# Kernel tuning notes

Hardware: AMD Instinct MI355X
Metric: run time of the kernel (lower is better)

## Reference

```python
import jax, jax.numpy as jnp
import numpy as np
import math


def _cnot_perm(n, c, t):
    # permutation on basis states implementing CNOT(control=c, target=t), qubit 0 = MSB
    idx = np.arange(2 ** n)
    ctrl = (idx >> (n - 1 - c)) & 1
    return np.where(ctrl == 1, idx ^ (1 << (n - 1 - t)), idx)


def _rot(phi, theta, omega):
    # PennyLane Rot(phi, theta, omega) = RZ(omega) RY(theta) RZ(phi)
    c = jnp.cos(theta / 2.0)
    s = jnp.sin(theta / 2.0)
    m00 = jnp.exp(-0.5j * (phi + omega)) * c
    m01 = -jnp.exp(0.5j * (phi - omega)) * s
    m10 = jnp.exp(-0.5j * (phi - omega)) * s
    m11 = jnp.exp(0.5j * (phi + omega)) * c
    return jnp.stack([jnp.stack([m00, m01]), jnp.stack([m10, m11])])


def _apply_1q(state, U, q, n):
    # apply 2x2 gate U on qubit q of an [N, 2^n] statevector
    N = state.shape[0]
    s = state.reshape(N, 2 ** q, 2, 2 ** (n - q - 1))
    s = jnp.einsum('ab,nqbr->nqar', U, s)
    return s.reshape(N, 2 ** n)


def reference(x, weights, bias, filter_size, strides):
    fs, st = int(filter_size), int(strides)
    B, C, H, W = x.shape
    Cout, L, n, _ = weights.shape
    oh = (H - fs) // st + 1
    ow = (W - fs) // st + 1

    # im2col / torch.unfold: [B,C,oh,fs,ow,fs] -> [B,oh,ow,C,fs,fs] -> [N, C*fs*fs]
    rows = (jnp.arange(oh) * st)[:, None] + jnp.arange(fs)[None, :]
    cols = (jnp.arange(ow) * st)[:, None] + jnp.arange(fs)[None, :]
    patches = x[:, :, rows][:, :, :, :, cols]                 # [B,C,oh,fs,ow,fs]
    patches = patches.transpose(0, 2, 4, 1, 3, 5).reshape(B * oh * ow, C * fs * fs)

    D = C * fs * fs
    dim = 2 ** n
    if D < dim:
        patches = jnp.pad(patches, ((0, 0), (0, dim - D)))

    # amplitude-encoding normalization; all-zero patch vectors are masked to 0 output
    norm = jnp.linalg.norm(patches, axis=-1, keepdims=True)
    nonzero = (norm[:, 0] > 0).astype(patches.dtype)          # [N]
    state0 = (patches / jnp.where(norm > 0, norm, 1.0)).astype(jnp.complex64)

    perms = [jnp.asarray(_cnot_perm(n, q, (q + 1) % n)) for q in range(n)]
    sign = (1.0 - 2.0 * ((jnp.arange(dim) >> (n - 1)) & 1)).astype(jnp.float32)  # Z on qubit 0

    def run_channel(wc):  # wc: [L, n, 3]
        state = state0
        for l in range(L):
            for q in range(n):
                state = _apply_1q(state, _rot(wc[l, q, 0], wc[l, q, 1], wc[l, q, 2]), q, n)
            if n > 1:
                for q in range(n):  # CNOT ring
                    state = state[:, perms[q]]
        return jnp.sum((jnp.abs(state) ** 2) * sign, axis=-1)  # [N] expval Z0

    exps = jax.vmap(run_channel)(weights)                     # [Cout, N]
    out = exps * nonzero[None, :] + bias[:, None]
    return out.reshape(Cout, B, oh, ow).transpose(1, 0, 2, 3)


def setup_inputs() -> dict:
    key = jax.random.key(0)
    k1, k2, k3 = jax.random.split(key, 3)
    B, Cin, H, W = 32, 16, 64, 64
    Cout, L, fs, st = 8, 3, 4, 2
    D = Cin * fs * fs
    n = math.ceil(math.log2(D))
    x = jax.random.normal(k1, (B, Cin, H, W), dtype=jnp.float32)
    weights = jax.random.normal(k2, (Cout, L, n, 3), dtype=jnp.float32)
    kk = 1.0 / D
    bias = jax.random.uniform(k3, (Cout,), minval=-math.sqrt(kk), maxval=math.sqrt(kk), dtype=jnp.float32)
    return {"x": x, "weights": weights, "bias": bias, "filter_size": fs, "strides": st}
```

## Files before the change

kernel.cpp:

```cpp
#include <hip/hip_runtime.h>
#include <math.h>

#define NQ     8
#define DIM    256
#define LAYERS 3
#define COUT   8
#define NB     32
#define OH     31
#define OW     31
#define NPATCH (NB*OH*OW)
#define NTILE8 32
#define PTOT   (NTILE8*1024)
#define NPTILE (PTOT/16)
#define NPAIR  72
#define MPACK  (NPAIR*64*8)
#define NWBLK  512

typedef _Float16 f16x8 __attribute__((ext_vector_type(8)));
typedef _Float16 f16x4 __attribute__((ext_vector_type(4)));
typedef _Float16 f16x2 __attribute__((ext_vector_type(2)));
typedef __fp16   h16x2 __attribute__((ext_vector_type(2)));
typedef float    f32x4 __attribute__((ext_vector_type(4)));

__device__ __constant__ unsigned char TI_OF_P[NPAIR] = {
    0,0,0,0,0,0,0,0, 1,1,1,1,1,1,1,1, 2,2,2,2,2,2,2, 3,3,3,3,3,3,3,
    4,4,4,4,4,4, 5,5,5,5,5,5, 6,6,6,6,6, 7,7,7,7,7, 8,8,8,8, 9,9,9,9,
    10,10,10, 11,11,11, 12,12, 13,13, 14, 15};
__device__ __constant__ unsigned char OFFT_C[16] =
    {0,8,16,23,30,36,42,47,52,56,60,63,66,68,70,71};

__device__ __forceinline__ float2 cmul(float2 a, float2 b) {
    return make_float2(a.x*b.x - a.y*b.y, a.x*b.y + a.y*b.x);
}
__device__ __forceinline__ float2 cadd(float2 a, float2 b) {
    return make_float2(a.x + b.x, a.y + b.y);
}

__device__ __forceinline__ int rho(int i) {
    #pragma unroll
    for (int q = 7; q >= 0; --q) {
        int t = (q + 1) & 7;
        if ((i >> (7 - q)) & 1) i ^= 1 << (7 - t);
    }
    return i;
}

__device__ __forceinline__ void gload_lds16(const _Float16* g, _Float16* l) {
    __builtin_amdgcn_global_load_lds(
        (const __attribute__((address_space(1))) void*)g,
        (__attribute__((address_space(3))) void*)l, 16, 0, 0);
}

__device__ __forceinline__ float fold4(f16x4 sv, f32x4 a, float o) {
    h16x2 s01 = __builtin_bit_cast(h16x2, (f16x2)__builtin_shufflevector(sv, sv, 0, 1));
    h16x2 s23 = __builtin_bit_cast(h16x2, (f16x2)__builtin_shufflevector(sv, sv, 2, 3));
    h16x2 y01 = __builtin_amdgcn_cvt_pkrtz(a[0], a[1]);
    h16x2 y23 = __builtin_amdgcn_cvt_pkrtz(a[2], a[3]);
    o = __builtin_amdgcn_fdot2(s01, y01, o, false);
    o = __builtin_amdgcn_fdot2(s23, y23, o, false);
    return o;
}

__device__ __forceinline__ float dpp_ror_add(float x, int ctrl) {
    int xi = __builtin_bit_cast(int, x);
    int yi;
    switch (ctrl) {
        case 0x128: yi = __builtin_amdgcn_update_dpp(0, xi, 0x128, 0xf, 0xf, true); break;
        case 0x124: yi = __builtin_amdgcn_update_dpp(0, xi, 0x124, 0xf, 0xf, true); break;
        case 0x122: yi = __builtin_amdgcn_update_dpp(0, xi, 0x122, 0xf, 0xf, true); break;
        default:    yi = __builtin_amdgcn_update_dpp(0, xi, 0x121, 0xf, 0xf, true); break;
    }
    return x + __builtin_bit_cast(float, yi);
}

__global__ __launch_bounds__(256) void wext(const float* __restrict__ w,
                                            _Float16* __restrict__ At,
                                            _Float16* __restrict__ Bt,
                                            const float* __restrict__ x,
                                            _Float16* __restrict__ sF) {
    __shared__ float2 g[96];
    __shared__ float2 vb[1024];
    __shared__ _Float16 sT[16][264];
    __shared__ float rsums[16][4];

    if (blockIdx.x < NWBLK) {
        const int ch  = blockIdx.x >> 6;
        const int wv  = threadIdx.x >> 6;
        const int l   = threadIdx.x & 63;
        const int col = (blockIdx.x & 63) * 4 + wv;

        if (threadIdx.x < 24) {
            const float* wp = w + (ch*24 + threadIdx.x)*3;
            float phi = wp[0], th = wp[1], om = wp[2];
            float cth = cosf(th * 0.5f), sth = sinf(th * 0.5f);
            float a = 0.5f * (phi + om), b = 0.5f * (phi - om);
            float sa, ca, sb, cb;
            sincosf(a, &sa, &ca);
            sincosf(b, &sb, &cb);
            g[threadIdx.x*4+0] = make_float2( cth*ca, -cth*sa);
            g[threadIdx.x*4+1] = make_float2(-sth*cb, -sth*sb);
            g[threadIdx.x*4+2] = make_float2( sth*cb, -sth*sb);
            g[threadIdx.x*4+3] = make_float2( cth*ca,  cth*sa);
        }
        __syncthreads();

        float2* vcol = vb + wv * 256;
        float2 v[4];
        #pragma unroll
        for (int k = 0; k < 4; ++k) {
            int r = l + 64*k;
            float2 acc = make_float2(1.f, 0.f);
            #pragma unroll
            for (int q = 0; q < 8; ++q) {
                int iq = (r >> (7 - q)) & 1, jq = (col >> (7 - q)) & 1;
                acc = cmul(acc, g[q*4 + iq*2 + jq]);
            }
            v[k] = acc;
        }

        #pragma unroll
        for (int lay = 1; lay < 3; ++lay) {
            #pragma unroll
            for (int k = 0; k < 4; ++k) vcol[l + 64*k] = v[k];
            #pragma unroll
            for (int k = 0; k < 4; ++k) v[k] = vcol[rho(l + 64*k)];
            {
                const float2 g0 = g[(lay*8+0)*4+0], g1 = g[(lay*8+0)*4+1];
                const float2 g2 = g[(lay*8+0)*4+2], g3 = g[(lay*8+0)*4+3];
                float2 nv[4];
                #pragma unroll
                for (int k = 0; k < 4; ++k) {
                    float2 xx = v[k], yy = v[k^2];
                    nv[k] = (k & 2) ? cadd(cmul(g2, yy), cmul(g3, xx))
                                    : cadd(cmul(g0, xx), cmul(g1, yy));
                }
                #pragma unroll
                for (int k = 0; k < 4; ++k) v[k] = nv[k];
            }
            {
                const float2 g0 = g[(lay*8+1)*4+0], g1 = g[(lay*8+1)*4+1];
                const float2 g2 = g[(lay*8+1)*4+2], g3 = g[(lay*8+1)*4+3];
                float2 nv[4];
                #pragma unroll
                for (int k = 0; k < 4; ++k) {
                    float2 xx = v[k], yy = v[k^1];
                    nv[k] = (k & 1) ? cadd(cmul(g2, yy), cmul(g3, xx))
                                    : cadd(cmul(g0, xx), cmul(g1, yy));
                }
                #pragma unroll
                for (int k = 0; k < 4; ++k) v[k] = nv[k];
            }
            #pragma unroll
            for (int q = 2; q < 8; ++q) {
                int bit = 1 << (7 - q);
                const float2 g0 = g[(lay*8+q)*4+0], g1 = g[(lay*8+q)*4+1];
                const float2 g2 = g[(lay*8+q)*4+2], g3 = g[(lay*8+q)*4+3];
                #pragma unroll
                for (int k = 0; k < 4; ++k) {
                    float2 yy;
                    yy.x = __shfl_xor(v[k].x, bit, 64);
                    yy.y = __shfl_xor(v[k].y, bit, 64);
                    float2 m0 = (l & bit) ? g3 : g0;
                    float2 m1 = (l & bit) ? g2 : g1;
                    v[k] = cadd(cmul(m0, v[k]), cmul(m1, yy));
                }
            }
        }
        #pragma unroll
        for (int k = 0; k < 4; ++k) vcol[l + 64*k] = v[k];
        #pragma unroll
        for (int k = 0; k < 4; ++k) v[k] = vcol[rho(l + 64*k)];

        size_t rowb = ((size_t)ch*256 + col) * 512;
        #pragma unroll
        for (int k = 0; k < 4; ++k) {
            int r = l + 64*k;
            float sgn = (r & 128) ? -1.f : 1.f;
            At[rowb + r]       = (_Float16)(sgn * v[k].x);
            At[rowb + 256 + r] = (_Float16)(sgn * v[k].y);
            Bt[rowb + r]       = (_Float16)v[k].x;
            Bt[rowb + 256 + r] = (_Float16)v[k].y;
        }
    } else {
        const int tb  = blockIdx.x - NWBLK;
        const int tid = threadIdx.x;
        const int wv  = tid >> 6, lane = tid & 63;

        float2 va[4], vc[4];
        #pragma unroll
        for (int pp = 0; pp < 4; ++pp) {
            int pl = wv*4 + pp;
            int p  = tb*16 + pl;
            float2 v01 = make_float2(0.f,0.f), v23 = make_float2(0.f,0.f);
            if (p < NPATCH) {
                int b = p / (OH*OW); int r = p % (OH*OW);
                int oi = r / OW, oj = r % OW;
                int ci = lane >> 2, fi = lane & 3;
                const float* xb = x + (((size_t)(b*16 + ci))*64 + (oi*2 + fi))*64 + oj*2;
                v01 = *(const float2*)xb;
                v23 = *(const float2*)(xb + 2);
            }
            va[pp] = v01; vc[pp] = v23;
            float ss = v01.x*v01.x + v01.y*v01.y + v23.x*v23.x + v23.y*v23.y;
            ss = dpp_ror_add(ss, 0x128);
            ss = dpp_ror_add(ss, 0x124);
            ss = dpp_ror_add(ss, 0x122);
            ss = dpp_ror_add(ss, 0x121);
            if ((lane & 15) == 0) rsums[pl][lane >> 4] = ss;
        }
        __syncthreads();

        #pragma unroll
        for (int pp = 0; pp < 4; ++pp) {
            int pl = wv*4 + pp;
            float tot = rsums[pl][0] + rsums[pl][1] + rsums[pl][2] + rsums[pl][3];
            float inv = tot > 0.f ? 1.f / sqrtf(tot) : 0.f;
            f16x4 o;
            o[0] = (_Float16)(va[pp].x*inv); o[1] = (_Float16)(va[pp].y*inv);
            o[2] = (_Float16)(vc[pp].x*inv); o[3] = (_Float16)(vc[pp].y*inv);
            *(f16x4*)&sT[pl][lane*4] = o;
        }
        __syncthreads();

        #pragma unroll
        for (int e = 0; e < 2; ++e) {
            int vi = tid + e*256;
            int ks = vi >> 6, ln = vi & 63;
            int kq = ln >> 4, prow = ln & 15;
            f16x8 o = *(const f16x8*)&sT[prow][ks*32 + kq*8];
            ((f16x8*)sF)[(size_t)tb*512 + vi] = o;
        }
    }
}

__global__ __launch_bounds__(256) __attribute__((amdgpu_waves_per_eu(1,4)))
void build_Mp(const _Float16* __restrict__ At,
              const _Float16* __restrict__ Bt,
              _Float16* __restrict__ Mp) {
    const int wv   = threadIdx.x >> 6;
    const int lane = threadIdx.x & 63;
    const int s    = blockIdx.x * 4 + wv;
    const int ch   = s / 144;
    const int r    = s % 144;
    const int p    = r >> 1;
    const int odd  = r & 1;
    const int ti   = TI_OF_P[p];
    const int jp   = p - OFFT_C[ti] + (ti >> 1);
    const int jt   = jp*2 + odd;
    const int c16  = lane & 15, kq = lane >> 4;
    _Float16* Mc = Mp + (size_t)ch * MPACK;

    f32x4 a0 = {0,0,0,0}, a1 = {0,0,0,0}, a2 = {0,0,0,0}, a3 = {0,0,0,0};
    if (jt >= ti) {
        const _Float16* Ar = At + ((size_t)ch*256 + ti*16 + c16) * 512 + kq*8;
        const _Float16* Br = Bt + ((size_t)ch*256 + jt*16 + c16) * 512 + kq*8;
        f16x8 af[16], bf[16];
        #pragma unroll
        for (int kk = 0; kk < 16; ++kk) {
            af[kk] = *(const f16x8*)(Ar + kk*32);
            bf[kk] = *(const f16x8*)(Br + kk*32);
        }
        #pragma unroll
        for (int kk = 0; kk < 16; kk += 4) {
            a0 = __builtin_amdgcn_mfma_f32_16x16x32_f16(af[kk+0], bf[kk+0], a0, 0, 0, 0);
            a1 = __builtin_amdgcn_mfma_f32_16x16x32_f16(af[kk+1], bf[kk+1], a1, 0, 0, 0);
            a2 = __builtin_amdgcn_mfma_f32_16x16x32_f16(af[kk+2], bf[kk+2], a2, 0, 0, 0);
            a3 = __builtin_amdgcn_mfma_f32_16x16x32_f16(af[kk+3], bf[kk+3], a3, 0, 0, 0);
        }
        a0 = a0 + a1 + a2 + a3;
    }

    const int wsel = odd * 16 + c16;
    const int kqp = wsel >> 3, jj = wsel & 7;
    #pragma unroll
    for (int reg = 0; reg < 4; ++reg) {
        int i_g = ti*16 + kq*4 + reg;
        int j_g = jt*16 + c16;
        float val = (jt >= ti) ? a0[reg] : 0.f;
        val *= (j_g > i_g) ? 2.f : ((j_g == i_g) ? 1.f : 0.f);
        Mc[(size_t)((p*64 + kqp*16 + (kq*4 + reg)) * 8 + jj)] = (_Float16)val;
    }
}

__global__ __attribute__((amdgpu_flat_work_group_size(1024,1024), amdgpu_waves_per_eu(2,4)))
void fusedqf(const _Float16* __restrict__ sF,
             const _Float16* __restrict__ Mp,
             const float* __restrict__ bias,
             float* __restrict__ out) {
    extern __shared__ _Float16 Mlds[];
    const int id   = blockIdx.x;
    const int xcd  = id & 7;
    const int g    = id >> 3;
    const int c    = g >> 2;
    const int tile = (g & 3) * 8 + xcd;
    const int tid  = threadIdx.x;
    const int lane = tid & 63;
    const int wv   = tid >> 6;
    const int prow = lane & 15, kq = lane >> 4;
    const int tp0  = tile*64 + wv*4;

    const _Float16* Msrc = Mp + (size_t)c * MPACK;
    if (wv < 8) {
        #pragma unroll
        for (int it = 0; it < 9; ++it) {
            int off = (wv*9 + it) * 512;
            gload_lds16(Msrc + off + lane*8, Mlds + off);
        }
    }

    f16x8 bfrag[4][4];
    #pragma unroll
    for (int pt = 0; pt < 4; ++pt) {
        const f16x8* src = (const f16x8*)sF + (size_t)(tp0 + pt)*512 + lane;
        #pragma unroll
        for (int ks = 0; ks < 4; ++ks)
            bfrag[pt][ks] = src[ks*64];
    }

    __syncthreads();

    const _Float16* fold0 = sF + ((size_t)tp0*512 + (kq>>1)*16 + prow)*8 + (kq&1)*4;
    float o0 = 0.f, o1 = 0.f, o2 = 0.f, o3 = 0.f;
    int pidx = 0;

    f16x4 svn[4];
    #pragma unroll
    for (int pt = 0; pt < 4; ++pt)
        svn[pt] = *(const f16x4*)(fold0 + pt*4096);

    #pragma unroll 1
    for (int t = 0; t < 8; ++t) {
        const int h = t >> 1;
        f16x4 svc[4];
        #pragma unroll
        for (int pt = 0; pt < 4; ++pt) svc[pt] = svn[pt];
        #pragma unroll
        for (int pt = 0; pt < 4; ++pt)
            svn[pt] = *(const f16x4*)(fold0 + pt*4096 + (t+1)*256);

        f32x4 a0 = {0,0,0,0}, a1 = {0,0,0,0}, a2 = {0,0,0,0}, a3 = {0,0,0,0};
        __builtin_amdgcn_s_setprio(1);
        #pragma unroll
        for (int ks = 0; ks < 4; ++ks) {
            if (ks >= h) {
                f16x8 m = *(const f16x8*)(Mlds + (size_t)pidx*512 + lane*8);
                a0 = __builtin_amdgcn_mfma_f32_16x16x32_f16(m, bfrag[0][ks], a0, 0, 0, 0);
                a1 = __builtin_amdgcn_mfma_f32_16x16x32_f16(m, bfrag[1][ks], a1, 0, 0, 0);
                a2 = __builtin_amdgcn_mfma_f32_16x16x32_f16(m, bfrag[2][ks], a2, 0, 0, 0);
                a3 = __builtin_amdgcn_mfma_f32_16x16x32_f16(m, bfrag[3][ks], a3, 0, 0, 0);
                ++pidx;
            }
        }
        __builtin_amdgcn_s_setprio(0);
        pidx += 4;

        o0 = fold4(svc[0], a0, o0);
        o1 = fold4(svc[1], a1, o1);
        o2 = fold4(svc[2], a2, o2);
        o3 = fold4(svc[3], a3, o3);
    }

    #pragma unroll
    for (int pt = 0; pt < 4; ++pt) {
        const f16x8* src = (const f16x8*)sF + (size_t)(tp0 + pt)*512 + lane;
        #pragma unroll
        for (int ks = 0; ks < 4; ++ks)
            bfrag[pt][ks] = src[(ks+4)*64];
    }

    pidx = 0;
    #pragma unroll
    for (int pt = 0; pt < 4; ++pt)
        svn[pt] = *(const f16x4*)(fold0 + pt*4096);

    #pragma unroll 1
    for (int t = 0; t < 16; ++t) {
        const int h = t >> 1;
        pidx += (h < 4) ? (4 - h) : 0;
        f16x4 svc[4];
        #pragma unroll
        for (int pt = 0; pt < 4; ++pt) svc[pt] = svn[pt];
        if (t < 15) {
            #pragma unroll
            for (int pt = 0; pt < 4; ++pt)
                svn[pt] = *(const f16x4*)(fold0 + pt*4096 + (t+1)*256);
        }

        f32x4 a0 = {0,0,0,0}, a1 = {0,0,0,0}, a2 = {0,0,0,0}, a3 = {0,0,0,0};
        __builtin_amdgcn_s_setprio(1);
        #pragma unroll
        for (int ks = 4; ks < 8; ++ks) {
            if (ks >= h) {
                f16x8 m = *(const f16x8*)(Mlds + (size_t)pidx*512 + lane*8);
                a0 = __builtin_amdgcn_mfma_f32_16x16x32_f16(m, bfrag[0][ks-4], a0, 0, 0, 0);
                a1 = __builtin_amdgcn_mfma_f32_16x16x32_f16(m, bfrag[1][ks-4], a1, 0, 0, 0);
                a2 = __builtin_amdgcn_mfma_f32_16x16x32_f16(m, bfrag[2][ks-4], a2, 0, 0, 0);
                a3 = __builtin_amdgcn_mfma_f32_16x16x32_f16(m, bfrag[3][ks-4], a3, 0, 0, 0);
                ++pidx;
            }
        }
        __builtin_amdgcn_s_setprio(0);

        o0 = fold4(svc[0], a0, o0);
        o1 = fold4(svc[1], a1, o1);
        o2 = fold4(svc[2], a2, o2);
        o3 = fold4(svc[3], a3, o3);
    }

    float ov[4] = {o0, o1, o2, o3};
    float bc = bias[c];
    #pragma unroll
    for (int pt = 0; pt < 4; ++pt) {
        float v = ov[pt];
        v += __shfl_xor(v, 16, 64);
        v += __shfl_xor(v, 32, 64);
        if (kq == 0) {
            int p = (tp0 + pt)*16 + prow;
            if (p < NPATCH) {
                int b = p / (OH*OW); int r2 = p % (OH*OW);
                int oi = r2 / OW, oj = r2 % OW;
                out[(((size_t)(b*COUT + c))*OH + oi)*OW + oj] = v + bc;
            }
        }
    }
}

extern "C" void kernel_launch(void* const* d_in, const int* in_sizes, int n_in,
                              void* d_out, int out_size, void* d_ws, size_t ws_size,
                              hipStream_t stream) {
    const float* x    = (const float*)d_in[0];
    const float* w    = (const float*)d_in[1];
    const float* bias = (const float*)d_in[2];
    float* out = (float*)d_out;

    const size_t OFF_AT  = 0;
    const size_t OFF_BT  = OFF_AT + 2097152;
    const size_t OFF_MP  = OFF_BT + 2097152;
    const size_t OFF_SF  = OFF_MP + 589824;
    const size_t TOTAL   = OFF_SF + 16777216;
    if (ws_size < TOTAL) return;

    char* ws = (char*)d_ws;
    _Float16* At = (_Float16*)(ws + OFF_AT);
    _Float16* Bt = (_Float16*)(ws + OFF_BT);
    _Float16* Mp = (_Float16*)(ws + OFF_MP);
    _Float16* sF = (_Float16*)(ws + OFF_SF);

    wext<<<NWBLK + NPTILE, 256, 0, stream>>>(w, At, Bt, x, sF);
    build_Mp<<<288, 256, 0, stream>>>(At, Bt, Mp);
    fusedqf<<<NTILE8*COUT, 1024, MPACK*sizeof(_Float16), stream>>>(sF, Mp, bias, out);
}
```

Baseline: 52.66 us.

## Merge two MFMA passes into one fully unrolled loop with register-resident fragments

Loads all eight B fragments and all sixteen fold state vectors into registers up front, then runs a single fully unrolled loop over row tiles in place of the two half-K passes. Each output tile now gets one accumulator sweep with no zero-padded skipped blocks and no second reload of B fragments or state vectors. The cost is a much larger register footprint (32 f16x8 plus 64 f16x4 per thread), which can lower occupancy or cause spills. The pair-index order in M changes from the earlier two-pass layout, so correctness relies on the packed M matching the new sequential order.

```diff
diff --git a/kernel.cpp b/kernel.cpp
--- a/kernel.cpp
+++ b/kernel.cpp
@@ -308,103 +308,45 @@
         }
     }
 
-    f16x8 bfrag[4][4];
+    f16x8 bfrag[4][8];
     #pragma unroll
     for (int pt = 0; pt < 4; ++pt) {
         const f16x8* src = (const f16x8*)sF + (size_t)(tp0 + pt)*512 + lane;
         #pragma unroll
-        for (int ks = 0; ks < 4; ++ks)
+        for (int ks = 0; ks < 8; ++ks)
             bfrag[pt][ks] = src[ks*64];
     }
+    const _Float16* fold0 = sF + ((size_t)tp0*512 + (kq>>1)*16 + prow)*8 + (kq&1)*4;
+    f16x4 sv[4][16];
+    #pragma unroll
+    for (int pt = 0; pt < 4; ++pt)
+        #pragma unroll
+        for (int t = 0; t < 16; ++t)
+            sv[pt][t] = *(const f16x4*)(fold0 + pt*4096 + t*256);
 
     __syncthreads();
 
-    const _Float16* fold0 = sF + ((size_t)tp0*512 + (kq>>1)*16 + prow)*8 + (kq&1)*4;
     float o0 = 0.f, o1 = 0.f, o2 = 0.f, o3 = 0.f;
     int pidx = 0;
 
-    f16x4 svn[4];
-    #pragma unroll
-    for (int pt = 0; pt < 4; ++pt)
-        svn[pt] = *(const f16x4*)(fold0 + pt*4096);
-
-    #pragma unroll 1
-    for (int t = 0; t < 8; ++t) {
-        const int h = t >> 1;
-        f16x4 svc[4];
-        #pragma unroll
-        for (int pt = 0; pt < 4; ++pt) svc[pt] = svn[pt];
-        #pragma unroll
-        for (int pt = 0; pt < 4; ++pt)
-            svn[pt] = *(const f16x4*)(fold0 + pt*4096 + (t+1)*256);
-
+    #pragma unroll
+    for (int t = 0; t < 16; ++t) {
         f32x4 a0 = {0,0,0,0}, a1 = {0,0,0,0}, a2 = {0,0,0,0}, a3 = {0,0,0,0};
         __builtin_amdgcn_s_setprio(1);
         #pragma unroll
-        for (int ks = 0; ks < 4; ++ks) {
-            if (ks >= h) {
-                f16x8 m = *(const f16x8*)(Mlds + (size_t)pidx*512 + lane*8);
-                a0 = __builtin_amdgcn_mfma_f32_16x16x32_f16(m, bfrag[0][ks], a0, 0, 0, 0);
-                a1 = __builtin_amdgcn_mfma_f32_16x16x32_f16(m, bfrag[1][ks], a1, 0, 0, 0);
-                a2 = __builtin_amdgcn_mfma_f32_16x16x32_f16(m, bfrag[2][ks], a2, 0, 0, 0);
-                a3 = __builtin_amdgcn_mfma_f32_16x16x32_f16(m, bfrag[3][ks], a3, 0, 0, 0);
-                ++pidx;
-            }
+        for (int ks = (t >> 1); ks < 8; ++ks) {
+            f16x8 m = *(const f16x8*)(Mlds + pidx*512 + lane*8);
+            a0 = __builtin_amdgcn_mfma_f32_16x16x32_f16(m, bfrag[0][ks], a0, 0, 0, 0);
+            a1 = __builtin_amdgcn_mfma_f32_16x16x32_f16(m, bfrag[1][ks], a1, 0, 0, 0);
+            a2 = __builtin_amdgcn_mfma_f32_16x16x32_f16(m, bfrag[2][ks], a2, 0, 0, 0);
+            a3 = __builtin_amdgcn_mfma_f32_16x16x32_f16(m, bfrag[3][ks], a3, 0, 0, 0);
+            ++pidx;
         }
         __builtin_amdgcn_s_setprio(0);
-        pidx += 4;
-
-        o0 = fold4(svc[0], a0, o0);
-        o1 = fold4(svc[1], a1, o1);
-        o2 = fold4(svc[2], a2, o2);
-        o3 = fold4(svc[3], a3, o3);
-    }
-
-    #pragma unroll
-    for (int pt = 0; pt < 4; ++pt) {
-        const f16x8* src = (const f16x8*)sF + (size_t)(tp0 + pt)*512 + lane;
-        #pragma unroll
-        for (int ks = 0; ks < 4; ++ks)
-            bfrag[pt][ks] = src[(ks+4)*64];
-    }
-
-    pidx = 0;
-    #pragma unroll
-    for (int pt = 0; pt < 4; ++pt)
-        svn[pt] = *(const f16x4*)(fold0 + pt*4096);
-
-    #pragma unroll 1
-    for (int t = 0; t < 16; ++t) {
-        const int h = t >> 1;
-        pidx += (h < 4) ? (4 - h) : 0;
-        f16x4 svc[4];
-        #pragma unroll
-        for (int pt = 0; pt < 4; ++pt) svc[pt] = svn[pt];
-        if (t < 15) {
-            #pragma unroll
-            for (int pt = 0; pt < 4; ++pt)
-                svn[pt] = *(const f16x4*)(fold0 + pt*4096 + (t+1)*256);
-        }
-
-        f32x4 a0 = {0,0,0,0}, a1 = {0,0,0,0}, a2 = {0,0,0,0}, a3 = {0,0,0,0};
-        __builtin_amdgcn_s_setprio(1);
-        #pragma unroll
-        for (int ks = 4; ks < 8; ++ks) {
-            if (ks >= h) {
-                f16x8 m = *(const f16x8*)(Mlds + (size_t)pidx*512 + lane*8);
-                a0 = __builtin_amdgcn_mfma_f32_16x16x32_f16(m, bfrag[0][ks-4], a0, 0, 0, 0);
-                a1 = __builtin_amdgcn_mfma_f32_16x16x32_f16(m, bfrag[1][ks-4], a1, 0, 0, 0);
-                a2 = __builtin_amdgcn_mfma_f32_16x16x32_f16(m, bfrag[2][ks-4], a2, 0, 0, 0);
-                a3 = __builtin_amdgcn_mfma_f32_16x16x32_f16(m, bfrag[3][ks-4], a3, 0, 0, 0);
-                ++pidx;
-            }
-        }
-        __builtin_amdgcn_s_setprio(0);
-
-        o0 = fold4(svc[0], a0, o0);
-        o1 = fold4(svc[1], a1, o1);
-        o2 = fold4(svc[2], a2, o2);
-        o3 = fold4(svc[3], a3, o3);
+        o0 = fold4(sv[0][t], a0, o0);
+        o1 = fold4(sv[1][t], a1, o1);
+        o2 = fold4(sv[2][t], a2, o2);
+        o3 = fold4(sv[3][t], a3, o3);
     }
 
     float ov[4] = {o0, o1, o2, o3};
```

Result: slower. 196.1 us (+272.4%).
